# Optimization experiments

Hardware: AMD Instinct MI355X
Metric: run time of the kernel (lower is better)

The kernel has to match this reference:

```python
import math
import jax, jax.numpy as jnp
import numpy as np

B, S, D = 4, 4096, 1024

def setup_inputs() -> dict:
    key = jax.random.key(0)
    ks = jax.random.split(key, 4)
    scale = 1.0 / math.sqrt(D)
    return {
        "x": jax.random.normal(ks[0], (B, S, D), dtype=jnp.float32),
        "Wq": jax.random.normal(ks[1], (D, D), dtype=jnp.float32) * scale,
        "bq": jnp.zeros((D,), dtype=jnp.float32),
        "Wk": jax.random.normal(ks[2], (D, D), dtype=jnp.float32) * scale,
        "bk": jnp.zeros((D,), dtype=jnp.float32),
        "Wv": jax.random.normal(ks[3], (D, D), dtype=jnp.float32) * scale,
        "bv": jnp.zeros((D,), dtype=jnp.float32),
    }

def reference(x, Wq, bq, Wk, bk, Wv, bv):
    # Linear layers (torch nn.Linear: x @ W.T + b)
    Q = jnp.einsum('bsd,ed->bse', x, Wq) + bq  # [B,S,D]
    K = jnp.einsum('bsd,ed->bse', x, Wk) + bk
    V = jnp.einsum('bsd,ed->bse', x, Wv) + bv
    # Full (non-flash) attention, scaled by sqrt(hidden_dim) as in source
    scores = jnp.einsum('bqd,bkd->bqk', Q, K) / jnp.sqrt(jnp.float32(Q.shape[-1]))
    attn = jax.nn.softmax(scores, axis=-1)  # [B,S,S]
    return jnp.einsum('bqk,bkd->bqd', attn, V)
```

## Files before the change

### kernel.cpp

```cpp
#include <hip/hip_runtime.h>
#include <hip/hip_bf16.h>
#include <stdint.h>


typedef __attribute__((ext_vector_type(4))) float f32x4;
typedef __attribute__((ext_vector_type(8))) short s16x8;
typedef __attribute__((ext_vector_type(4))) unsigned short u16x4;
typedef unsigned int u32;
typedef unsigned short u16;

__device__ __forceinline__ u16 f2b(float f) {
  u32 u = __float_as_uint(f);
  u = (u + 0x7FFFu + ((u >> 16) & 1u)) >> 16;
  return (u16)u;
}
__device__ __forceinline__ float b2f(u16 h) {
  return __uint_as_float(((u32)h) << 16);
}

__device__ __forceinline__ void gload_lds16(const void* g, void* l) {
  __builtin_amdgcn_global_load_lds(
      (const __attribute__((address_space(1))) void*)(const void*)g,
      (__attribute__((address_space(3))) void*)(void*)l, 16, 0, 0);
}

#define BARRIER() asm volatile("s_barrier" ::: "memory")
#define WAITLGKM0() asm volatile("s_waitcnt lgkmcnt(0)" ::: "memory")
#define WAITVM(N) asm volatile("s_waitcnt vmcnt(" #N ")" ::: "memory")

__global__ __launch_bounds__(256) void k_cvt(const float* __restrict__ in,
                                             u16* __restrict__ out, int n4) {
  int i = blockIdx.x * 256 + threadIdx.x;
  if (i >= n4) return;
  f32x4 f = ((const f32x4*)in)[i];
  u16x4 h;
#pragma unroll
  for (int j = 0; j < 4; ++j) h[j] = f2b(f[j]);
  ((u16x4*)out)[i] = h;
}

template <int MODE>
__global__ __launch_bounds__(512)
void k_gemm256(const u16* __restrict__ A, const u16* __restrict__ B, int lda,
               int ldb, int K, const float* __restrict__ bias,
               const float* __restrict__ biasB, void* __restrict__ Cv, int ldc,
               float scale, size_t az, size_t bz, size_t czb,
               float* __restrict__ part) {
  extern __shared__ __align__(16) u16 lds[];

  A += (size_t)blockIdx.z * az;
  B += (size_t)blockIdx.z * bz;
  char* C = (char*)Cv + (size_t)blockIdx.z * czb;
  const float* bi = (MODE == 0 && blockIdx.z != 0) ? biasB : bias;

  const int gx = gridDim.x;
  const int nwg = gx * gridDim.y;
  const int bid = blockIdx.y * gx + blockIdx.x;
  const int q = nwg >> 3, r = nwg & 7;
  const int xcd = bid & 7, idx = bid >> 3;
  const int tile = (xcd < r ? xcd * (q + 1) : r * (q + 1) + (xcd - r) * q) + idx;
  const int m0 = (tile / gx) * 256;
  const int n0 = (tile % gx) * 256;

  const int tid = threadIdx.x;
  const int lane = tid & 63;
  const int wid = tid >> 6;
  const int wm = wid >> 2;
  const int wn = wid & 3;

  const int srow = lane >> 3;
  const int gcol = (((lane & 7) ^ srow) << 3);
  const int rA = lane & 15;
  const int kq = (lane >> 4) << 3;
  const int xr = (lane & 7) << 3;

#define STAGE_A(h, kt, b)                                                    \
  do {                                                                       \
    _Pragma("unroll") for (int j = 0; j < 2; ++j)                            \
        gload_lds16(A + (size_t)(m0 + (h)*128 + j * 64 + wid * 8 + srow) *   \
                            lda + (kt)*64 + gcol,                            \
                    &lds[(b)*32768 + (h)*8192 + j * 4096 + wid * 512]);      \
  } while (0)
#define STAGE_B(h, kt, b)                                                    \
  do {                                                                       \
    _Pragma("unroll") for (int j = 0; j < 2; ++j)                            \
        gload_lds16(B + (size_t)(n0 + (h)*128 + j * 64 + wid * 8 + srow) *   \
                            ldb + (kt)*64 + gcol,                            \
                    &lds[(b)*32768 + 16384 + (h)*8192 + j * 4096 +           \
                         wid * 512]);                                        \
  } while (0)
#define RD_A(dst, b, sub)                                                    \
  do {                                                                       \
    _Pragma("unroll") for (int mi = 0; mi < 4; ++mi)                         \
        _Pragma("unroll") for (int ks = 0; ks < 2; ++ks)                     \
            dst[mi][ks] = *(const s16x8*)&lds[(b)*32768 +                    \
                (wm * 128 + (sub) + mi * 16 + rA) * 64 +                     \
                ((ks * 32 + kq) ^ xr)];                                      \
  } while (0)
#define RD_B(dst, b, sub)                                                    \
  do {                                                                       \
    _Pragma("unroll") for (int ni = 0; ni < 2; ++ni)                         \
        _Pragma("unroll") for (int ks = 0; ks < 2; ++ks)                     \
            dst[ni][ks] = *(const s16x8*)&lds[(b)*32768 + 16384 +            \
                (wn * 64 + (sub) + ni * 16 + rA) * 64 +                      \
                ((ks * 32 + kq) ^ xr)];                                      \
  } while (0)
#define MM(AF, BF, MO, NO)                                                   \
  do {                                                                       \
    _Pragma("unroll") for (int mi = 0; mi < 4; ++mi)                         \
        _Pragma("unroll") for (int ni = 0; ni < 2; ++ni)                     \
            _Pragma("unroll") for (int ks = 0; ks < 2; ++ks)                 \
                acc[(MO) + mi][(NO) + ni] =                                  \
                    __builtin_amdgcn_mfma_f32_16x16x32_bf16(                 \
                        AF[mi][ks], BF[ni][ks], acc[(MO) + mi][(NO) + ni],   \
                        0, 0, 0);                                            \
  } while (0)

  f32x4 acc[8][4] = {};
  const int NT = K >> 6;

  STAGE_A(0, 0, 0);
  STAGE_A(1, 0, 0);
  STAGE_B(0, 0, 0);
  STAGE_B(1, 0, 0);
  if (NT > 1) {
    STAGE_A(0, 1, 1);
    STAGE_A(1, 1, 1);
    STAGE_B(0, 1, 1);
    STAGE_B(1, 1, 1);
    WAITVM(8);
  } else {
    WAITVM(0);
  }
  BARRIER();

  s16x8 af0[4][2], af1[4][2], bf0[2][2], bf1[2][2];
  for (int t = 0; t < NT; ++t) {
    const int b = t & 1;
    RD_A(af0, b, 0);
    RD_B(bf0, b, 0);
    RD_A(af1, b, 64);
    RD_B(bf1, b, 32);
    __builtin_amdgcn_s_setprio(1);
    MM(af0, bf0, 0, 0);
    MM(af1, bf0, 4, 0);
    MM(af0, bf1, 0, 2);
    MM(af1, bf1, 4, 2);
    __builtin_amdgcn_s_setprio(0);
    WAITLGKM0();
    BARRIER();
    if (t + 2 < NT) {
      STAGE_A(0, t + 2, b);
      STAGE_A(1, t + 2, b);
      STAGE_B(0, t + 2, b);
      STAGE_B(1, t + 2, b);
      WAITVM(8);
      BARRIER();
    } else if (t + 1 < NT) {
      WAITVM(0);
      BARRIER();
    }
  }

  float* fl = (float*)lds;
  float* rinv = fl + 16640;
  const int l15 = lane & 15;
  const int r4 = (lane >> 4) * 4;
  f32x4 bcol4 = {0.f, 0.f, 0.f, 0.f};
  if (MODE == 0) bcol4 = *(const f32x4*)&bi[n0 + lane * 4];
  if (MODE == 3) {
    if (tid < 256) {
      const float* pr = &part[((size_t)blockIdx.z * 4096 + m0 + tid) * 16];
      float s = 0.f;
#pragma unroll
      for (int j = 0; j < 4; ++j) {
        f32x4 t4 = *(const f32x4*)&pr[j * 4];
        s += (t4[0] + t4[1]) + (t4[2] + t4[3]);
      }
      rinv[tid] = 1.0f / s;
    }
  }
#pragma unroll
  for (int c = 0; c < 4; ++c) {
    __syncthreads();
    if (wm == (c >> 1)) {
      const int mibase = (c & 1) * 4;
#pragma unroll
      for (int mi = 0; mi < 4; ++mi) {
#pragma unroll
        for (int nj = 0; nj < 4; ++nj) {
          const int col = wn * 64 + nj * 16 + l15;
          const int rbase = mi * 16 + r4;
#pragma unroll
          for (int rr = 0; rr < 4; ++rr) {
            float v = acc[mibase + mi][nj][rr];
            if (MODE == 2) v = __expf(v * scale);
            fl[(rbase + rr) * 260 + col] = v;
          }
        }
      }
    }
    __syncthreads();
#pragma unroll
    for (int p = 0; p < 8; ++p) {
      const int rl = p * 8 + wid;
      const int rowg = m0 + c * 64 + rl;
      f32x4 v = *(const f32x4*)&fl[rl * 260 + lane * 4];
      if (MODE == 0) {
#pragma unroll
        for (int j = 0; j < 4; ++j) v[j] += bcol4[j];
        u16x4 h;
#pragma unroll
        for (int j = 0; j < 4; ++j) h[j] = f2b(v[j]);
        ((u16x4*)((u16*)C + (size_t)rowg * ldc + n0))[lane] = h;
      } else if (MODE == 1) {
        const float br = bi[rowg];
        u16x4 h;
#pragma unroll
        for (int j = 0; j < 4; ++j) h[j] = f2b(v[j] + br);
        ((u16x4*)((u16*)C + (size_t)rowg * ldc + n0))[lane] = h;
      } else if (MODE == 2) {
        u16x4 h;
#pragma unroll
        for (int j = 0; j < 4; ++j) h[j] = f2b(v[j]);
        ((u16x4*)((u16*)C + (size_t)rowg * ldc + n0))[lane] = h;
      } else {
        const float iv = rinv[c * 64 + rl];
#pragma unroll
        for (int j = 0; j < 4; ++j) v[j] *= iv;
        ((f32x4*)((float*)C + (size_t)rowg * ldc + n0))[lane] = v;
      }
    }
    if (MODE == 2) {
      const int row8 = tid >> 3;
      const int seg = tid & 7;
      const float* rp = &fl[row8 * 260 + seg * 32];
      f32x4 s4 = {0.f, 0.f, 0.f, 0.f};
#pragma unroll
      for (int j = 0; j < 8; ++j) {
        f32x4 t4 = *(const f32x4*)&rp[j * 4];
#pragma unroll
        for (int d = 0; d < 4; ++d) s4[d] += t4[d];
      }
      float s = (s4[0] + s4[1]) + (s4[2] + s4[3]);
      s += __shfl_xor(s, 1, 64);
      s += __shfl_xor(s, 2, 64);
      s += __shfl_xor(s, 4, 64);
      if (seg == 0)
        part[((size_t)blockIdx.z * 4096 + m0 + c * 64 + row8) * 16 +
             (n0 >> 8)] = s;
    }
  }
#undef STAGE_A
#undef STAGE_B
#undef RD_A
#undef RD_B
#undef MM
}

extern "C" void kernel_launch(void* const* d_in, const int* in_sizes, int n_in,
                              void* d_out, int out_size, void* d_ws,
                              size_t ws_size, hipStream_t stream) {
  const float* x = (const float*)d_in[0];
  const float* Wq = (const float*)d_in[1];
  const float* bq = (const float*)d_in[2];
  const float* Wk = (const float*)d_in[3];
  const float* bk = (const float*)d_in[4];
  const float* Wv = (const float*)d_in[5];
  const float* bv = (const float*)d_in[6];
  float* out = (float*)d_out;
  char* ws = (char*)d_ws;

  const size_t MB = 1ull << 20;
  u16* Qb = (u16*)(ws + 0 * MB);
  u16* Kb = (u16*)(ws + 32 * MB);
  u16* VtAll = (u16*)(ws + 64 * MB);
  u16* Xb = (u16*)(ws + 96 * MB);
  u16* Sc = (u16*)(ws + 96 * MB);
  u16* Wqb = (u16*)(ws + 224 * MB);
  u16* Wkb = Wqb + 1048576;
  u16* Wvb = Wqb + 2097152;
  float* part = (float*)(ws + 231 * MB);

  hipFuncSetAttribute((const void*)k_gemm256<0>,
                      hipFuncAttributeMaxDynamicSharedMemorySize, 131072);
  hipFuncSetAttribute((const void*)k_gemm256<1>,
                      hipFuncAttributeMaxDynamicSharedMemorySize, 131072);
  hipFuncSetAttribute((const void*)k_gemm256<2>,
                      hipFuncAttributeMaxDynamicSharedMemorySize, 131072);
  hipFuncSetAttribute((const void*)k_gemm256<3>,
                      hipFuncAttributeMaxDynamicSharedMemorySize, 131072);

  k_cvt<<<16384, 256, 0, stream>>>(x, Xb, 4194304);
  k_cvt<<<1024, 256, 0, stream>>>(Wq, Wqb, 262144);
  k_cvt<<<1024, 256, 0, stream>>>(Wk, Wkb, 262144);
  k_cvt<<<1024, 256, 0, stream>>>(Wv, Wvb, 262144);

  dim3 blk(512);
  const size_t LDSB = 131072;
  k_gemm256<0><<<dim3(4, 64, 2), blk, LDSB, stream>>>(
      Xb, Wqb, 1024, 1024, 1024, bq, bk, Qb, 1024, 1.f, 0, 1048576,
      (size_t)32 * MB, nullptr);
  k_gemm256<1><<<dim3(64, 4, 1), blk, LDSB, stream>>>(
      Wvb, Xb, 1024, 1024, 1024, bv, nullptr, VtAll, 16384, 1.f, 0, 0, 0,
      nullptr);
  k_gemm256<2><<<dim3(16, 16, 4), blk, LDSB, stream>>>(
      Qb, Kb, 1024, 1024, 1024, nullptr, nullptr, Sc, 4096, 0.03125f, 4194304,
      4194304, (size_t)4096 * 4096 * 2, part);
  k_gemm256<3><<<dim3(4, 16, 4), blk, LDSB, stream>>>(
      Sc, VtAll, 4096, 16384, 4096, nullptr, nullptr, out, 1024, 1.f, 16777216,
      4096, (size_t)4096 * 1024 * 4, part);
}
```

Measured before the change: 425.5 us.

## Interleave LDS reads, MFMA clusters and global prefetch in four-phase GEMM k-loop

Splits each k-tile into four phases, each a smaller LDS fragment read followed by a barrier-fenced MFMA cluster. The next tile's global-to-LDS staging for A and B is issued between those clusters instead of after all the math. The loop is unrolled by two so the double-buffer index is a compile-time constant. The goal is to overlap memory traffic with matrix-core work and keep MFMA fed. The cost is many more barriers per tile, and the code now assumes the tile count is even and at least two.

After: 414.9 us. 2.5% less time.

```diff
diff --git a/kernel.cpp b/kernel.cpp
--- a/kernel.cpp
+++ b/kernel.cpp
@@ -123,44 +123,66 @@
   STAGE_A(1, 0, 0);
   STAGE_B(0, 0, 0);
   STAGE_B(1, 0, 0);
-  if (NT > 1) {
-    STAGE_A(0, 1, 1);
-    STAGE_A(1, 1, 1);
-    STAGE_B(0, 1, 1);
-    STAGE_B(1, 1, 1);
-    WAITVM(8);
-  } else {
-    WAITVM(0);
+  STAGE_A(0, 1, 1);
+  STAGE_A(1, 1, 1);
+  STAGE_B(0, 1, 1);
+  STAGE_B(1, 1, 1);
+  WAITVM(8);
+  BARRIER();
+
+  s16x8 af0[4][2], af1[4][2], bf0[2][2], bf1[2][2];
+
+#define KTILE(b, tt)                                                         \
+  do {                                                                       \
+                                                                    \
+    RD_A(af0, b, 0);                                                         \
+    RD_B(bf0, b, 0);                                                         \
+    BARRIER();                                                               \
+    WAITLGKM0();                                                             \
+    __builtin_amdgcn_s_setprio(1);                                           \
+    MM(af0, bf0, 0, 0);                                                      \
+    __builtin_amdgcn_s_setprio(0);                                           \
+    BARRIER();                                                               \
+                                                      \
+    RD_A(af1, b, 64);                                                        \
+    BARRIER();                                                               \
+    WAITLGKM0();                                                             \
+    __builtin_amdgcn_s_setprio(1);                                           \
+    MM(af1, bf0, 4, 0);                                                      \
+    __builtin_amdgcn_s_setprio(0);                                           \
+    BARRIER();                              \
+                          \
+    RD_B(bf1, b, 32);                                                        \
+    if ((tt) + 2 < NT) {                                                     \
+      STAGE_A(0, (tt) + 2, b);                                               \
+      STAGE_A(1, (tt) + 2, b);                                               \
+    }                                                                        \
+    BARRIER();                                                               \
+    WAITLGKM0();                                                             \
+    __builtin_amdgcn_s_setprio(1);                                           \
+    MM(af0, bf1, 0, 2);                                                      \
+    __builtin_amdgcn_s_setprio(0);                                           \
+    BARRIER();                              \
+                  \
+    if ((tt) + 2 < NT) {                                                     \
+      STAGE_B(0, (tt) + 2, b);                                               \
+      STAGE_B(1, (tt) + 2, b);                                               \
+      WAITVM(8);                                                             \
+    } else if ((tt) + 1 < NT) {                                              \
+      WAITVM(0);                                                             \
+    }                                                                        \
+    BARRIER();                                                               \
+    __builtin_amdgcn_s_setprio(1);                                           \
+    MM(af1, bf1, 4, 2);                                                      \
+    __builtin_amdgcn_s_setprio(0);                                           \
+    BARRIER();                                                               \
+  } while (0)
+
+  for (int t = 0; t < NT; t += 2) {
+    KTILE(0, t);
+    KTILE(1, t + 1);
   }
-  BARRIER();
-
-  s16x8 af0[4][2], af1[4][2], bf0[2][2], bf1[2][2];
-  for (int t = 0; t < NT; ++t) {
-    const int b = t & 1;
-    RD_A(af0, b, 0);
-    RD_B(bf0, b, 0);
-    RD_A(af1, b, 64);
-    RD_B(bf1, b, 32);
-    __builtin_amdgcn_s_setprio(1);
-    MM(af0, bf0, 0, 0);
-    MM(af1, bf0, 4, 0);
-    MM(af0, bf1, 0, 2);
-    MM(af1, bf1, 4, 2);
-    __builtin_amdgcn_s_setprio(0);
-    WAITLGKM0();
-    BARRIER();
-    if (t + 2 < NT) {
-      STAGE_A(0, t + 2, b);
-      STAGE_A(1, t + 2, b);
-      STAGE_B(0, t + 2, b);
-      STAGE_B(1, t + 2, b);
-      WAITVM(8);
-      BARRIER();
-    } else if (t + 1 < NT) {
-      WAITVM(0);
-      BARRIER();
-    }
-  }
+#undef KTILE
 
   float* fl = (float*)lds;
   float* rinv = fl + 16640;
```
